# Kernel optimization log

Hardware: AMD Instinct MI355X
Metric: run time of the kernel (lower is better)

## Reference

```python
import jax, jax.numpy as jnp
import numpy as np

B = 8192
NUM_NODES = 100000
EMB = 128
W1D, W2D, W3D = 64, 128, 256   # witness_dims
CODE = 128
HID = 64                        # hardcoded hidden_dim in WitnessExtractor / decoder
TOTW = W1D + W2D + W3D          # 448


def _linear_params(key, fan_in, fan_out):
    k1, k2 = jax.random.split(key)
    bound = 1.0 / np.sqrt(fan_in)
    w = jax.random.uniform(k1, (fan_out, fan_in), jnp.float32, -bound, bound)
    b = jax.random.uniform(k2, (fan_out,), jnp.float32, -bound, bound)
    return w, b


def setup_inputs() -> dict:
    key = jax.random.key(0)
    ks = jax.random.split(key, 12)
    u = jax.random.randint(ks[0], (B,), 0, NUM_NODES, dtype=jnp.int64 if jax.config.jax_enable_x64 else jnp.int32)
    v = jax.random.randint(ks[1], (B,), 0, NUM_NODES, dtype=u.dtype)
    emb = jax.random.normal(ks[2], (NUM_NODES, EMB), jnp.float32)
    e1_w1, e1_b1 = _linear_params(ks[3], 2 * EMB, HID)
    e1_w2, e1_b2 = _linear_params(ks[4], HID, W1D)
    e2_w1, e2_b1 = _linear_params(ks[5], 2 * EMB + W1D, HID)
    e2_w2, e2_b2 = _linear_params(ks[6], HID, W2D)
    e3_w1, e3_b1 = _linear_params(ks[7], 2 * EMB + W2D, HID)
    e3_w2, e3_b2 = _linear_params(ks[8], HID, W3D)
    trop_w = jax.random.normal(ks[9], (CODE, TOTW), jnp.float32)  # init_scale=1.0
    dec_w1, dec_b1 = _linear_params(ks[10], CODE, HID)
    dec_w2, dec_b2 = _linear_params(ks[11], HID, 1)
    return dict(u=u, v=v, emb=emb,
                e1_w1=e1_w1, e1_b1=e1_b1, e1_w2=e1_w2, e1_b2=e1_b2,
                e2_w1=e2_w1, e2_b1=e2_b1, e2_w2=e2_w2, e2_b2=e2_b2,
                e3_w1=e3_w1, e3_b1=e3_b1, e3_w2=e3_w2, e3_b2=e3_b2,
                trop_w=trop_w, dec_w1=dec_w1, dec_b1=dec_b1,
                dec_w2=dec_w2, dec_b2=dec_b2)


def _witness(x, w1, b1, w2, b2):
    h = jax.nn.relu(x @ w1.T + b1)
    return jax.nn.sigmoid(h @ w2.T + b2)


def reference(u, v, emb,
              e1_w1, e1_b1, e1_w2, e1_b2,
              e2_w1, e2_b1, e2_w2, e2_b2,
              e3_w1, e3_b1, e3_w2, e3_b2,
              trop_w, dec_w1, dec_b1, dec_w2, dec_b2):
    u_emb = emb[u]                               # [B, EMB]
    v_emb = emb[v]
    base = jnp.concatenate([u_emb, v_emb], axis=1)  # [B, 2*EMB]
    w1 = _witness(base, e1_w1, e1_b1, e1_w2, e1_b2)
    w2 = _witness(jnp.concatenate([base, w1], axis=1), e2_w1, e2_b1, e2_w2, e2_b2)
    w3 = _witness(jnp.concatenate([base, w2], axis=1), e3_w1, e3_b1, e3_w2, e3_b2)
    wit = jnp.concatenate([w1, w2, w3], axis=1)  # [B, TOTW]
    # tropical (min-plus) matmul: code[b,o] = min_j (wit[b,j] + trop_w[o,j])
    code = jnp.min(wit[:, None, :] + trop_w[None, :, :], axis=2)  # [B, CODE]
    h = jax.nn.relu(code @ dec_w1.T + dec_b1)
    return h @ dec_w2.T + dec_b2                 # [B, 1]
```

## Files before the change

kernel.cpp:

```cpp
#include <hip/hip_runtime.h>
#include <hip/hip_fp16.h>
#include <math.h>

#define BATCH 8192
#define EMB 128
#define TILE 16
#define NTHREADS 1024
#define NWAVES 16
#define CH 136
#define SLOT 32

#define OFF_E1W1 0
#define OFF_E1W2 16384
#define OFF_E2W1 20480
#define OFF_E2W2 40960
#define OFF_E3W1 49152
#define OFF_E3W2 73728
#define OFF_DW1  90112
#define OFF_DW2  98304
#define W_DENSE  98368

typedef __attribute__((ext_vector_type(8))) _Float16 v8h;
typedef __attribute__((ext_vector_type(4))) float v4f;

struct Smem {
    _Float16 XB[32 * CH];
    _Float16 WC[56 * CH];
    _Float16 H[8 * CH];
    _Float16 CODE[16 * CH];
    unsigned int ent[128 * SLOT];
    unsigned int cnt[128];
};

__global__ __launch_bounds__(1024) void prep_kernel(
    const float* __restrict__ s0, const float* __restrict__ s1,
    const float* __restrict__ s2, const float* __restrict__ s3,
    const float* __restrict__ s4, const float* __restrict__ s5,
    const float* __restrict__ s6, const float* __restrict__ s7,
    const float* __restrict__ trop, _Float16* __restrict__ ws)
{
    const int b = blockIdx.x;
    const int tid = threadIdx.x;
    if (b < 25) {
        const int idx4 = (b * 1024 + tid) * 4;
        if (idx4 >= W_DENSE) return;
        const float* src; int off;
        if      (idx4 < OFF_E1W2) { src = s0; off = OFF_E1W1; }
        else if (idx4 < OFF_E2W1) { src = s1; off = OFF_E1W2; }
        else if (idx4 < OFF_E2W2) { src = s2; off = OFF_E2W1; }
        else if (idx4 < OFF_E3W1) { src = s3; off = OFF_E2W2; }
        else if (idx4 < OFF_E3W2) { src = s4; off = OFF_E3W1; }
        else if (idx4 < OFF_DW1)  { src = s5; off = OFF_E3W2; }
        else if (idx4 < OFF_DW2)  { src = s6; off = OFF_DW1;  }
        else                      { src = s7; off = OFF_DW2;  }
        const float4 v = *(const float4*)(src + (idx4 - off));
        _Float16* dst = ws + idx4;
        dst[0] = (_Float16)v.x; dst[1] = (_Float16)v.y;
        dst[2] = (_Float16)v.z; dst[3] = (_Float16)v.w;
    } else {
        const int lane = tid & 63;
        const int wave = tid >> 6;
        const int o = (b - 25) * 16 + wave;
        if (o >= 128) return;
        unsigned int* base = (unsigned int*)(ws + W_DENSE);

        const float* row = trop + (size_t)o * 448;
        float vals[7];
        float mn = 1e30f;
        #pragma unroll
        for (int it = 0; it < 7; ++it) {
            vals[it] = row[lane + it * 64];
            mn = fminf(mn, vals[it]);
        }
        mn = fminf(mn, __shfl_xor(mn, 1, 64));
        mn = fminf(mn, __shfl_xor(mn, 2, 64));
        mn = fminf(mn, __shfl_xor(mn, 4, 64));
        mn = fminf(mn, __shfl_xor(mn, 8, 64));
        mn = fminf(mn, __shfl_xor(mn, 16, 64));
        mn = fminf(mn, __shfl_xor(mn, 32, 64));
        const float thr = mn + 1.02f;

        const unsigned long long ltmask = (1ull << lane) - 1ull;
        unsigned int pos0 = 0;
        #pragma unroll
        for (int it = 0; it < 7; ++it) {
            const bool sel = vals[it] <= thr;
            const unsigned long long m = __ballot(sel);
            if (sel) {
                const unsigned int pos = pos0 + (unsigned)__popcll(m & ltmask);
                if (pos < SLOT) {
                    const unsigned short hb =
                        __builtin_bit_cast(unsigned short, (_Float16)vals[it]);
                    base[o * SLOT + pos] = ((unsigned)(lane + it * 64) << 16) | hb;
                }
            }
            pos0 += (unsigned)__popcll(m);
        }
        if (lane == 0) base[4096 + o] = pos0;
    }
}

template <int K, int O, int ACT>
__device__ __forceinline__ void dense_job(
    const _Float16* __restrict__ Wg, const float* __restrict__ bias,
    const _Float16* A0, _Float16* OutC, int jid, int lane)
{
    constexpr int STEPS = K / 32;
    static_assert(STEPS % 2 == 0, "even steps");
    const int l15 = lane & 15;
    const int quad = lane >> 4;
    const int o = jid * 16 + l15;
    const _Float16* wrow = Wg + (size_t)o * K + quad * 8;
    v4f c0 = {0.f, 0.f, 0.f, 0.f};
    v4f c1 = {0.f, 0.f, 0.f, 0.f};
    #pragma unroll
    for (int s = 0; s < STEPS; s += 2) {
        const v8h a0 = *(const v8h*)(A0 + (s * 4 + quad) * CH + l15 * 8);
        const v8h b0 = *(const v8h*)(wrow + s * 32);
        const v8h a1 = *(const v8h*)(A0 + ((s + 1) * 4 + quad) * CH + l15 * 8);
        const v8h b1 = *(const v8h*)(wrow + (s + 1) * 32);
        c0 = __builtin_amdgcn_mfma_f32_16x16x32_f16(a0, b0, c0, 0, 0, 0);
        c1 = __builtin_amdgcn_mfma_f32_16x16x32_f16(a1, b1, c1, 0, 0, 0);
    }
    const v4f c = c0 + c1;
    const float bs = bias[o];
    #pragma unroll
    for (int i = 0; i < 4; ++i) {
        float vv = c[i] + bs;
        if (ACT == 0) vv = fmaxf(vv, 0.f);
        else          vv = 1.f / (1.f + __expf(-vv));
        const int m = quad * 4 + i;
        OutC[(o >> 3) * CH + m * 8 + (o & 7)] = (_Float16)vv;
    }
}

template <int KW, int RS>
__device__ __forceinline__ void addpb_job(
    const _Float16* __restrict__ Wg, const _Float16* A0,
    const v4f hold, _Float16* OutH, int jid, int lane)
{
    constexpr int STEPS = KW / 32;
    static_assert(STEPS % 2 == 0, "even steps");
    const int l15 = lane & 15;
    const int quad = lane >> 4;
    const int o = jid * 16 + l15;
    const _Float16* wrow = Wg + (size_t)o * RS + quad * 8;
    v4f c0 = hold;
    v4f c1 = {0.f, 0.f, 0.f, 0.f};
    #pragma unroll
    for (int s = 0; s < STEPS; s += 2) {
        const v8h a0 = *(const v8h*)(A0 + (s * 4 + quad) * CH + l15 * 8);
        const v8h b0 = *(const v8h*)(wrow + s * 32);
        const v8h a1 = *(const v8h*)(A0 + ((s + 1) * 4 + quad) * CH + l15 * 8);
        const v8h b1 = *(const v8h*)(wrow + (s + 1) * 32);
        c0 = __builtin_amdgcn_mfma_f32_16x16x32_f16(a0, b0, c0, 0, 0, 0);
        c1 = __builtin_amdgcn_mfma_f32_16x16x32_f16(a1, b1, c1, 0, 0, 0);
    }
    const v4f c = c0 + c1;
    #pragma unroll
    for (int i = 0; i < 4; ++i) {
        const float vv = fmaxf(c[i], 0.f);
        const int m = quad * 4 + i;
        OutH[(o >> 3) * CH + m * 8 + (o & 7)] = (_Float16)vv;
    }
}

__global__ __launch_bounds__(NTHREADS, 8) void tacit_fused_kernel(
    const int* __restrict__ u, const int* __restrict__ v,
    const float* __restrict__ emb,
    const float* __restrict__ e1_b1, const float* __restrict__ e1_b2,
    const float* __restrict__ e2_b1, const float* __restrict__ e2_b2,
    const float* __restrict__ e3_b1, const float* __restrict__ e3_b2,
    const float* __restrict__ dec_b1, const float* __restrict__ dec_b2,
    const float* __restrict__ trop,
    const _Float16* __restrict__ ws,
    float* __restrict__ out)
{
    __shared__ Smem S;
    const int tid = threadIdx.x;
    const int lane = tid & 63;
    const int wave = tid >> 6;
    const int row0 = blockIdx.x * TILE;

    {
        const unsigned int* base = (const unsigned int*)(ws + W_DENSE);
        *(uint4*)&S.ent[tid * 4] = *(const uint4*)(base + tid * 4);
        if (tid < 32) *(uint4*)&S.cnt[tid * 4] = *(const uint4*)(base + 4096 + tid * 4);
    }
    if (tid < 512) {
        const int row = tid & 15;
        const int kq = tid >> 4;
        const int node = (kq < 16) ? u[row0 + row] : v[row0 + row];
        const int col = (kq & 15) * 8;
        const float4 f0 = *(const float4*)(emb + (size_t)node * EMB + col);
        const float4 f1 = *(const float4*)(emb + (size_t)node * EMB + col + 4);
        v8h hv;
        hv[0] = (_Float16)f0.x; hv[1] = (_Float16)f0.y;
        hv[2] = (_Float16)f0.z; hv[3] = (_Float16)f0.w;
        hv[4] = (_Float16)f1.x; hv[5] = (_Float16)f1.y;
        hv[6] = (_Float16)f1.z; hv[7] = (_Float16)f1.w;
        *(v8h*)&S.XB[kq * CH + row * 8] = hv;
    }
    __syncthreads();

    v4f hold = {0.f, 0.f, 0.f, 0.f};
    if (wave < 12) {
        const int tgt = wave >> 2;
        const int nt  = wave & 3;
        const int l15 = lane & 15;
        const int quad = lane >> 4;
        const int o = nt * 16 + l15;
        const _Float16* wrow;
        const float* bias;
        if (tgt == 0)      { wrow = ws + OFF_E1W1 + (size_t)o * 256; bias = e1_b1; }
        else if (tgt == 1) { wrow = ws + OFF_E2W1 + (size_t)o * 320; bias = e2_b1; }
        else               { wrow = ws + OFF_E3W1 + (size_t)o * 384; bias = e3_b1; }
        wrow += quad * 8;
        v4f c0 = {0.f, 0.f, 0.f, 0.f};
        v4f c1 = {0.f, 0.f, 0.f, 0.f};
        #pragma unroll
        for (int s = 0; s < 8; s += 2) {
            const v8h a0 = *(const v8h*)(S.XB + (s * 4 + quad) * CH + l15 * 8);
            const v8h b0 = *(const v8h*)(wrow + s * 32);
            const v8h a1 = *(const v8h*)(S.XB + ((s + 1) * 4 + quad) * CH + l15 * 8);
            const v8h b1v = *(const v8h*)(wrow + (s + 1) * 32);
            c0 = __builtin_amdgcn_mfma_f32_16x16x32_f16(a0, b0, c0, 0, 0, 0);
            c1 = __builtin_amdgcn_mfma_f32_16x16x32_f16(a1, b1v, c1, 0, 0, 0);
        }
        const v4f c = c0 + c1;
        const float bs = bias[o];
        if (tgt == 0) {
            #pragma unroll
            for (int i = 0; i < 4; ++i) {
                const float vv = fmaxf(c[i] + bs, 0.f);
                S.H[(o >> 3) * CH + (quad * 4 + i) * 8 + (o & 7)] = (_Float16)vv;
            }
        } else {
            #pragma unroll
            for (int i = 0; i < 4; ++i) hold[i] = c[i] + bs;
        }
    }
    __syncthreads();

    if (wave < 4)
        dense_job<64, 64, 1>(ws + OFF_E1W2, e1_b2, S.H, S.WC, wave, lane);
    __syncthreads();

    if (wave >= 4 && wave < 8)
        addpb_job<64, 320>(ws + OFF_E2W1 + 256, S.WC, hold, S.H, wave - 4, lane);
    __syncthreads();

    {
        const int dnt = (wave < 4) ? wave : (wave >= 12 ? wave - 8 : -1);
        if (dnt >= 0)
            dense_job<64, 128, 1>(ws + OFF_E2W2, e2_b2, S.H, S.WC + 8 * CH, dnt, lane);
    }
    __syncthreads();

    if (wave >= 8 && wave < 12)
        addpb_job<128, 384>(ws + OFF_E3W1 + 256, S.WC + 8 * CH, hold, S.H, wave - 8, lane);
    __syncthreads();

    dense_job<64, 256, 1>(ws + OFF_E3W2, e3_b2, S.H, S.WC + 24 * CH, wave, lane);
    __syncthreads();

    {
        const int r = lane & 15;
        const int cp = lane >> 4;
        const _Float16* wr8 = &S.WC[r * 8];
        float acc[8];
        int idx[8], end8[8];
        #pragma unroll
        for (int i = 0; i < 8; ++i) {
            const int o = (wave << 3) + i;
            const int n = (int)S.cnt[o];
            idx[i] = o * SLOT + cp;
            end8[i] = o * SLOT + (n < SLOT ? n : SLOT);
            acc[i] = 1e30f;
        }
        bool any = true;
        while (any) {
            any = false;
            #pragma unroll
            for (int i = 0; i < 8; ++i) {
                if (idx[i] < end8[i]) {
                    const unsigned int cwv = S.ent[idx[i]];
                    const int j = (int)(cwv >> 16);
                    const float tv = (float)__builtin_bit_cast(
                        _Float16, (unsigned short)(cwv & 0xffffu));
                    acc[i] = fminf(acc[i], (float)wr8[(j >> 3) * CH + (j & 7)] + tv);
                    idx[i] += 4;
                    any = true;
                }
            }
        }
        #pragma unroll
        for (int i = 0; i < 8; ++i) {
            const int o = (wave << 3) + i;
            if ((int)S.cnt[o] > SLOT) {
                const float* trow = trop + (size_t)o * 448;
                for (int j = cp; j < 448; j += 4)
                    acc[i] = fminf(acc[i], (float)wr8[(j >> 3) * CH + (j & 7)] + trow[j]);
            }
        }
        #pragma unroll
        for (int i = 0; i < 8; ++i) {
            float a = acc[i];
            a = fminf(a, __shfl_xor(a, 16, 64));
            a = fminf(a, __shfl_xor(a, 32, 64));
            if (cp == 0) {
                const int o = (wave << 3) + i;
                S.CODE[(o >> 3) * CH + r * 8 + (o & 7)] = (_Float16)a;
            }
        }
    }
    __syncthreads();

    if (wave < 4)
        dense_job<128, 64, 0>(ws + OFF_DW1, dec_b1, S.CODE, S.H, wave, lane);
    __syncthreads();

    if (tid < 64) {
        const int r = lane & 15;
        const int part = lane >> 4;
        const _Float16* w2 = ws + OFF_DW2;
        float s = 0.f;
        #pragma unroll
        for (int q = 0; q < 2; ++q) {
            const int c = part + q * 4;
            const v8h hr = *(const v8h*)(&S.H[c * CH + r * 8]);
            const v8h wr = *(const v8h*)(w2 + c * 8);
            #pragma unroll
            for (int t = 0; t < 8; ++t) s += (float)hr[t] * (float)wr[t];
        }
        s += __shfl_xor(s, 16, 64);
        s += __shfl_xor(s, 32, 64);
        if (part == 0) out[row0 + r] = s + dec_b2[0];
    }
}

extern "C" void kernel_launch(void* const* d_in, const int* in_sizes, int n_in,
                              void* d_out, int out_size, void* d_ws, size_t ws_size,
                              hipStream_t stream) {
    const int*   u      = (const int*)d_in[0];
    const int*   v      = (const int*)d_in[1];
    const float* emb    = (const float*)d_in[2];
    const float* e1_w1  = (const float*)d_in[3];
    const float* e1_b1  = (const float*)d_in[4];
    const float* e1_w2  = (const float*)d_in[5];
    const float* e1_b2  = (const float*)d_in[6];
    const float* e2_w1  = (const float*)d_in[7];
    const float* e2_b1  = (const float*)d_in[8];
    const float* e2_w2  = (const float*)d_in[9];
    const float* e2_b2  = (const float*)d_in[10];
    const float* e3_w1  = (const float*)d_in[11];
    const float* e3_b1  = (const float*)d_in[12];
    const float* e3_w2  = (const float*)d_in[13];
    const float* e3_b2  = (const float*)d_in[14];
    const float* trop_w = (const float*)d_in[15];
    const float* dec_w1 = (const float*)d_in[16];
    const float* dec_b1 = (const float*)d_in[17];
    const float* dec_w2 = (const float*)d_in[18];
    const float* dec_b2 = (const float*)d_in[19];
    float* out = (float*)d_out;
    _Float16* ws = (_Float16*)d_ws;

    prep_kernel<<<33, 1024, 0, stream>>>(
        e1_w1, e1_w2, e2_w1, e2_w2, e3_w1, e3_w2, dec_w1, dec_w2, trop_w, ws);

    tacit_fused_kernel<<<BATCH / TILE, NTHREADS, 0, stream>>>(
        u, v, emb,
        e1_b1, e1_b2, e2_b1, e2_b2, e3_b1, e3_b2, dec_b1, dec_b2,
        trop_w, ws, out);
}
```

Baseline: 151.5 us.

## Process two 16-row tiles per block and read sparse tropical entries from global

Each 1024-thread block now handles 32 batch rows as two 16-row sub-tiles, so waves that sat idle in the chained witness stages get work on the second tile. The grid is halved and the base GEMMs, dense jobs and decoder are redistributed across all 16 waves. The sparse tropical entry table is no longer staged into LDS and is read from global or L2 instead, and XB and CODE share a union to keep LDS size in check. The trade-off is more serial work per block, fewer blocks, and global-latency loads in the min-plus loop.

After: 163.9 us. +8.2%, slower.

```diff
diff --git a/kernel.cpp b/kernel.cpp
--- a/kernel.cpp
+++ b/kernel.cpp
@@ -4,7 +4,6 @@
 
 #define BATCH 8192
 #define EMB 128
-#define TILE 16
 #define NTHREADS 1024
 #define NWAVES 16
 #define CH 136
@@ -24,12 +23,12 @@
 typedef __attribute__((ext_vector_type(4))) float v4f;
 
 struct Smem {
-    _Float16 XB[32 * CH];
-    _Float16 WC[56 * CH];
-    _Float16 H[8 * CH];
-    _Float16 CODE[16 * CH];
-    unsigned int ent[128 * SLOT];
-    unsigned int cnt[128];
+    union {
+        _Float16 XB[2][32 * CH];
+        _Float16 CODE[2][16 * CH];
+    } U;
+    _Float16 WC[2][56 * CH];
+    _Float16 H[2][8 * CH];
 };
 
 __global__ __launch_bounds__(1024) void prep_kernel(
@@ -129,9 +128,40 @@
         float vv = c[i] + bs;
         if (ACT == 0) vv = fmaxf(vv, 0.f);
         else          vv = 1.f / (1.f + __expf(-vv));
-        const int m = quad * 4 + i;
-        OutC[(o >> 3) * CH + m * 8 + (o & 7)] = (_Float16)vv;
-    }
+        OutC[(o >> 3) * CH + (quad * 4 + i) * 8 + (o & 7)] = (_Float16)vv;
+    }
+}
+
+__device__ __forceinline__ v4f base_gemm(
+    const _Float16* __restrict__ ws, const _Float16* XB, int tgt, int nt,
+    int lane, const float* __restrict__ b1, const float* __restrict__ b2,
+    const float* __restrict__ b3)
+{
+    const int l15 = lane & 15;
+    const int quad = lane >> 4;
+    const int o = nt * 16 + l15;
+    const _Float16* wrow;
+    const float* bias;
+    if (tgt == 0)      { wrow = ws + OFF_E1W1 + (size_t)o * 256; bias = b1; }
+    else if (tgt == 1) { wrow = ws + OFF_E2W1 + (size_t)o * 320; bias = b2; }
+    else               { wrow = ws + OFF_E3W1 + (size_t)o * 384; bias = b3; }
+    wrow += quad * 8;
+    v4f c0 = {0.f, 0.f, 0.f, 0.f};
+    v4f c1 = {0.f, 0.f, 0.f, 0.f};
+    #pragma unroll
+    for (int s = 0; s < 8; s += 2) {
+        const v8h a0 = *(const v8h*)(XB + (s * 4 + quad) * CH + l15 * 8);
+        const v8h b0 = *(const v8h*)(wrow + s * 32);
+        const v8h a1 = *(const v8h*)(XB + ((s + 1) * 4 + quad) * CH + l15 * 8);
+        const v8h b1v = *(const v8h*)(wrow + (s + 1) * 32);
+        c0 = __builtin_amdgcn_mfma_f32_16x16x32_f16(a0, b0, c0, 0, 0, 0);
+        c1 = __builtin_amdgcn_mfma_f32_16x16x32_f16(a1, b1v, c1, 0, 0, 0);
+    }
+    v4f c = c0 + c1;
+    const float bs = bias[o];
+    #pragma unroll
+    for (int i = 0; i < 4; ++i) c[i] += bs;
+    return c;
 }
 
 template <int KW, int RS>
@@ -160,8 +190,7 @@
     #pragma unroll
     for (int i = 0; i < 4; ++i) {
         const float vv = fmaxf(c[i], 0.f);
-        const int m = quad * 4 + i;
-        OutH[(o >> 3) * CH + m * 8 + (o & 7)] = (_Float16)vv;
+        OutH[(o >> 3) * CH + (quad * 4 + i) * 8 + (o & 7)] = (_Float16)vv;
     }
 }
 
@@ -180,17 +209,14 @@
     const int tid = threadIdx.x;
     const int lane = tid & 63;
     const int wave = tid >> 6;
-    const int row0 = blockIdx.x * TILE;
+    const int row0 = blockIdx.x * 32;
 
     {
-        const unsigned int* base = (const unsigned int*)(ws + W_DENSE);
-        *(uint4*)&S.ent[tid * 4] = *(const uint4*)(base + tid * 4);
-        if (tid < 32) *(uint4*)&S.cnt[tid * 4] = *(const uint4*)(base + 4096 + tid * 4);
-    }
-    if (tid < 512) {
-        const int row = tid & 15;
-        const int kq = tid >> 4;
-        const int node = (kq < 16) ? u[row0 + row] : v[row0 + row];
+        const int t   = tid >> 9;
+        const int t9  = tid & 511;
+        const int row = t9 & 15;
+        const int kq  = t9 >> 4;
+        const int node = (kq < 16) ? u[row0 + t * 16 + row] : v[row0 + t * 16 + row];
         const int col = (kq & 15) * 8;
         const float4 f0 = *(const float4*)(emb + (size_t)node * EMB + col);
         const float4 f1 = *(const float4*)(emb + (size_t)node * EMB + col + 4);
@@ -199,128 +225,135 @@
         hv[2] = (_Float16)f0.z; hv[3] = (_Float16)f0.w;
         hv[4] = (_Float16)f1.x; hv[5] = (_Float16)f1.y;
         hv[6] = (_Float16)f1.z; hv[7] = (_Float16)f1.w;
-        *(v8h*)&S.XB[kq * CH + row * 8] = hv;
-    }
-    __syncthreads();
-
-    v4f hold = {0.f, 0.f, 0.f, 0.f};
-    if (wave < 12) {
-        const int tgt = wave >> 2;
-        const int nt  = wave & 3;
+        *(v8h*)&S.U.XB[t][kq * CH + row * 8] = hv;
+    }
+    __syncthreads();
+
+    v4f hold_a = {0.f, 0.f, 0.f, 0.f};
+    v4f hold_b = {0.f, 0.f, 0.f, 0.f};
+    {
         const int l15 = lane & 15;
         const int quad = lane >> 4;
-        const int o = nt * 16 + l15;
-        const _Float16* wrow;
-        const float* bias;
-        if (tgt == 0)      { wrow = ws + OFF_E1W1 + (size_t)o * 256; bias = e1_b1; }
-        else if (tgt == 1) { wrow = ws + OFF_E2W1 + (size_t)o * 320; bias = e2_b1; }
-        else               { wrow = ws + OFF_E3W1 + (size_t)o * 384; bias = e3_b1; }
-        wrow += quad * 8;
-        v4f c0 = {0.f, 0.f, 0.f, 0.f};
-        v4f c1 = {0.f, 0.f, 0.f, 0.f};
-        #pragma unroll
-        for (int s = 0; s < 8; s += 2) {
-            const v8h a0 = *(const v8h*)(S.XB + (s * 4 + quad) * CH + l15 * 8);
-            const v8h b0 = *(const v8h*)(wrow + s * 32);
-            const v8h a1 = *(const v8h*)(S.XB + ((s + 1) * 4 + quad) * CH + l15 * 8);
-            const v8h b1v = *(const v8h*)(wrow + (s + 1) * 32);
-            c0 = __builtin_amdgcn_mfma_f32_16x16x32_f16(a0, b0, c0, 0, 0, 0);
-            c1 = __builtin_amdgcn_mfma_f32_16x16x32_f16(a1, b1v, c1, 0, 0, 0);
-        }
-        const v4f c = c0 + c1;
-        const float bs = bias[o];
-        if (tgt == 0) {
+        if (wave < 12) {
+            const int tgt = wave >> 2;
+            const v4f c = base_gemm(ws, S.U.XB[0], tgt, wave & 3, lane,
+                                    e1_b1, e2_b1, e3_b1);
+            if (tgt == 0) {
+                const int o = (wave & 3) * 16 + l15;
+                #pragma unroll
+                for (int i = 0; i < 4; ++i)
+                    S.H[0][(o >> 3) * CH + (quad * 4 + i) * 8 + (o & 7)] =
+                        (_Float16)fmaxf(c[i], 0.f);
+            } else {
+                hold_a = c;
+            }
+        } else {
+            const v4f c = base_gemm(ws, S.U.XB[1], 0, wave & 3, lane,
+                                    e1_b1, e2_b1, e3_b1);
+            const int o = (wave & 3) * 16 + l15;
             #pragma unroll
-            for (int i = 0; i < 4; ++i) {
-                const float vv = fmaxf(c[i] + bs, 0.f);
-                S.H[(o >> 3) * CH + (quad * 4 + i) * 8 + (o & 7)] = (_Float16)vv;
-            }
-        } else {
-            #pragma unroll
-            for (int i = 0; i < 4; ++i) hold[i] = c[i] + bs;
-        }
-    }
-    __syncthreads();
-
-    if (wave < 4)
-        dense_job<64, 64, 1>(ws + OFF_E1W2, e1_b2, S.H, S.WC, wave, lane);
+            for (int i = 0; i < 4; ++i)
+                S.H[1][(o >> 3) * CH + (quad * 4 + i) * 8 + (o & 7)] =
+                    (_Float16)fmaxf(c[i], 0.f);
+        }
+        if (wave < 8) {
+            hold_b = base_gemm(ws, S.U.XB[1], (wave >> 2) + 1, wave & 3, lane,
+                               e1_b1, e2_b1, e3_b1);
+        }
+    }
+    __syncthreads();
+
+    if (wave >= 8)
+        dense_job<64, 64, 1>(ws + OFF_E1W2, e1_b2, S.H[(wave - 8) >> 2],
+                             S.WC[(wave - 8) >> 2], (wave - 8) & 3, lane);
     __syncthreads();
 
     if (wave >= 4 && wave < 8)
-        addpb_job<64, 320>(ws + OFF_E2W1 + 256, S.WC, hold, S.H, wave - 4, lane);
+        addpb_job<64, 320>(ws + OFF_E2W1 + 256, S.WC[0], hold_a, S.H[0], wave - 4, lane);
+    else if (wave < 4)
+        addpb_job<64, 320>(ws + OFF_E2W1 + 256, S.WC[1], hold_b, S.H[1], wave, lane);
+    __syncthreads();
+
+    dense_job<64, 128, 1>(ws + OFF_E2W2, e2_b2, S.H[wave >> 3],
+                          S.WC[wave >> 3] + 8 * CH, wave & 7, lane);
+    __syncthreads();
+
+    if (wave >= 8 && wave < 12)
+        addpb_job<128, 384>(ws + OFF_E3W1 + 256, S.WC[0] + 8 * CH, hold_a,
+                            S.H[0], wave - 8, lane);
+    else if (wave >= 4 && wave < 8)
+        addpb_job<128, 384>(ws + OFF_E3W1 + 256, S.WC[1] + 8 * CH, hold_b,
+                            S.H[1], wave - 4, lane);
+    __syncthreads();
+
+    dense_job<64, 256, 1>(ws + OFF_E3W2, e3_b2, S.H[0], S.WC[0] + 24 * CH, wave, lane);
+    dense_job<64, 256, 1>(ws + OFF_E3W2, e3_b2, S.H[1], S.WC[1] + 24 * CH, wave, lane);
     __syncthreads();
 
     {
-        const int dnt = (wave < 4) ? wave : (wave >= 12 ? wave - 8 : -1);
-        if (dnt >= 0)
-            dense_job<64, 128, 1>(ws + OFF_E2W2, e2_b2, S.H, S.WC + 8 * CH, dnt, lane);
-    }
-    __syncthreads();
-
-    if (wave >= 8 && wave < 12)
-        addpb_job<128, 384>(ws + OFF_E3W1 + 256, S.WC + 8 * CH, hold, S.H, wave - 8, lane);
-    __syncthreads();
-
-    dense_job<64, 256, 1>(ws + OFF_E3W2, e3_b2, S.H, S.WC + 24 * CH, wave, lane);
-    __syncthreads();
-
-    {
+        const unsigned int* entg = (const unsigned int*)(ws + W_DENSE);
+        const unsigned int* cntg = entg + 4096;
         const int r = lane & 15;
         const int cp = lane >> 4;
-        const _Float16* wr8 = &S.WC[r * 8];
-        float acc[8];
-        int idx[8], end8[8];
-        #pragma unroll
-        for (int i = 0; i < 8; ++i) {
-            const int o = (wave << 3) + i;
-            const int n = (int)S.cnt[o];
-            idx[i] = o * SLOT + cp;
-            end8[i] = o * SLOT + (n < SLOT ? n : SLOT);
-            acc[i] = 1e30f;
-        }
-        bool any = true;
-        while (any) {
-            any = false;
+        #pragma unroll 1
+        for (int t = 0; t < 2; ++t) {
+            const _Float16* wr8 = &S.WC[t][r * 8];
+            float acc[8];
+            int idx8[8], end8[8];
             #pragma unroll
             for (int i = 0; i < 8; ++i) {
-                if (idx[i] < end8[i]) {
-                    const unsigned int cwv = S.ent[idx[i]];
-                    const int j = (int)(cwv >> 16);
-                    const float tv = (float)__builtin_bit_cast(
-                        _Float16, (unsigned short)(cwv & 0xffffu));
-                    acc[i] = fminf(acc[i], (float)wr8[(j >> 3) * CH + (j & 7)] + tv);
-                    idx[i] += 4;
-                    any = true;
+                const int o = (wave << 3) + i;
+                const int n = (int)cntg[o];
+                idx8[i] = o * SLOT + cp;
+                end8[i] = o * SLOT + (n < SLOT ? n : SLOT);
+                acc[i] = 1e30f;
+            }
+            bool any = true;
+            while (any) {
+                any = false;
+                #pragma unroll
+                for (int i = 0; i < 8; ++i) {
+                    if (idx8[i] < end8[i]) {
+                        const unsigned int cwv = entg[idx8[i]];
+                        const int j = (int)(cwv >> 16);
+                        const float tv = (float)__builtin_bit_cast(
+                            _Float16, (unsigned short)(cwv & 0xffffu));
+                        acc[i] = fminf(acc[i], (float)wr8[(j >> 3) * CH + (j & 7)] + tv);
+                        idx8[i] += 4;
+                        any = true;
+                    }
                 }
             }
-        }
-        #pragma unroll
-        for (int i = 0; i < 8; ++i) {
-            const int o = (wave << 3) + i;
-            if ((int)S.cnt[o] > SLOT) {
-                const float* trow = trop + (size_t)o * 448;
-                for (int j = cp; j < 448; j += 4)
-                    acc[i] = fminf(acc[i], (float)wr8[(j >> 3) * CH + (j & 7)] + trow[j]);
-            }
-        }
-        #pragma unroll
-        for (int i = 0; i < 8; ++i) {
-            float a = acc[i];
-            a = fminf(a, __shfl_xor(a, 16, 64));
-            a = fminf(a, __shfl_xor(a, 32, 64));
-            if (cp == 0) {
+            #pragma unroll
+            for (int i = 0; i < 8; ++i) {
                 const int o = (wave << 3) + i;
-                S.CODE[(o >> 3) * CH + r * 8 + (o & 7)] = (_Float16)a;
-            }
-        }
-    }
-    __syncthreads();
-
-    if (wave < 4)
-        dense_job<128, 64, 0>(ws + OFF_DW1, dec_b1, S.CODE, S.H, wave, lane);
-    __syncthreads();
-
-    if (tid < 64) {
+                if ((int)cntg[o] > SLOT) {
+                    const float* trow = trop + (size_t)o * 448;
+                    for (int j = cp; j < 448; j += 4)
+                        acc[i] = fminf(acc[i],
+                                       (float)wr8[(j >> 3) * CH + (j & 7)] + trow[j]);
+                }
+            }
+            #pragma unroll
+            for (int i = 0; i < 8; ++i) {
+                float a = acc[i];
+                a = fminf(a, __shfl_xor(a, 16, 64));
+                a = fminf(a, __shfl_xor(a, 32, 64));
+                if (cp == 0) {
+                    const int o = (wave << 3) + i;
+                    S.U.CODE[t][(o >> 3) * CH + r * 8 + (o & 7)] = (_Float16)a;
+                }
+            }
+        }
+    }
+    __syncthreads();
+
+    if (wave < 8)
+        dense_job<128, 64, 0>(ws + OFF_DW1, dec_b1, S.U.CODE[wave >> 2],
+                              S.H[wave >> 2], wave & 3, lane);
+    __syncthreads();
+
+    if (wave < 2) {
         const int r = lane & 15;
         const int part = lane >> 4;
         const _Float16* w2 = ws + OFF_DW2;
@@ -328,14 +361,14 @@
         #pragma unroll
         for (int q = 0; q < 2; ++q) {
             const int c = part + q * 4;
-            const v8h hr = *(const v8h*)(&S.H[c * CH + r * 8]);
+            const v8h hr = *(const v8h*)(&S.H[wave][c * CH + r * 8]);
             const v8h wr = *(const v8h*)(w2 + c * 8);
             #pragma unroll
             for (int t = 0; t < 8; ++t) s += (float)hr[t] * (float)wr[t];
         }
         s += __shfl_xor(s, 16, 64);
         s += __shfl_xor(s, 32, 64);
-        if (part == 0) out[row0 + r] = s + dec_b2[0];
+        if (part == 0) out[row0 + wave * 16 + r] = s + dec_b2[0];
     }
 }
 
@@ -368,7 +401,7 @@
     prep_kernel<<<33, 1024, 0, stream>>>(
         e1_w1, e1_w2, e2_w1, e2_w2, e3_w1, e3_w2, dec_w1, dec_w2, trop_w, ws);
 
-    tacit_fused_kernel<<<BATCH / TILE, NTHREADS, 0, stream>>>(
+    tacit_fused_kernel<<<BATCH / 32, NTHREADS, 0, stream>>>(
         u, v, emb,
         e1_b1, e1_b2, e2_b1, e2_b2, e3_b1, e3_b2, dec_b1, dec_b2,
         trop_w, ws, out);
```

## Drop prep kernel and build sparse tropical table inside fused kernel

Applied to the files above, without the earlier changes.

Removes the separate prep launch: each block now builds the pruned tropical-weight entry list itself, spreading the row builds across waves that are idle during the witness MLP stages. Dense weights are read as fp32 and converted to fp16 on the fly instead of from a prebuilt fp16 workspace. The XB and CODE buffers share LDS through a union. This trades a kernel launch and its serial dependency for redundant per-block trop reads from L2 and extra conversion work in the GEMM loops.

Result: slower. 172.0 us (+13.5%).

```diff
diff --git a/kernel.cpp b/kernel.cpp
--- a/kernel.cpp
+++ b/kernel.cpp
@@ -10,99 +10,73 @@
 #define CH 136
 #define SLOT 32
 
-#define OFF_E1W1 0
-#define OFF_E1W2 16384
-#define OFF_E2W1 20480
-#define OFF_E2W2 40960
-#define OFF_E3W1 49152
-#define OFF_E3W2 73728
-#define OFF_DW1  90112
-#define OFF_DW2  98304
-#define W_DENSE  98368
-
 typedef __attribute__((ext_vector_type(8))) _Float16 v8h;
 typedef __attribute__((ext_vector_type(4))) float v4f;
 
 struct Smem {
-    _Float16 XB[32 * CH];
+    union {
+        _Float16 XB[32 * CH];
+        _Float16 CODE[16 * CH];
+    } U;
     _Float16 WC[56 * CH];
     _Float16 H[8 * CH];
-    _Float16 CODE[16 * CH];
     unsigned int ent[128 * SLOT];
     unsigned int cnt[128];
 };
 
-__global__ __launch_bounds__(1024) void prep_kernel(
-    const float* __restrict__ s0, const float* __restrict__ s1,
-    const float* __restrict__ s2, const float* __restrict__ s3,
-    const float* __restrict__ s4, const float* __restrict__ s5,
-    const float* __restrict__ s6, const float* __restrict__ s7,
-    const float* __restrict__ trop, _Float16* __restrict__ ws)
-{
-    const int b = blockIdx.x;
-    const int tid = threadIdx.x;
-    if (b < 25) {
-        const int idx4 = (b * 1024 + tid) * 4;
-        if (idx4 >= W_DENSE) return;
-        const float* src; int off;
-        if      (idx4 < OFF_E1W2) { src = s0; off = OFF_E1W1; }
-        else if (idx4 < OFF_E2W1) { src = s1; off = OFF_E1W2; }
-        else if (idx4 < OFF_E2W2) { src = s2; off = OFF_E2W1; }
-        else if (idx4 < OFF_E3W1) { src = s3; off = OFF_E2W2; }
-        else if (idx4 < OFF_E3W2) { src = s4; off = OFF_E3W1; }
-        else if (idx4 < OFF_DW1)  { src = s5; off = OFF_E3W2; }
-        else if (idx4 < OFF_DW2)  { src = s6; off = OFF_DW1;  }
-        else                      { src = s7; off = OFF_DW2;  }
-        const float4 v = *(const float4*)(src + (idx4 - off));
-        _Float16* dst = ws + idx4;
-        dst[0] = (_Float16)v.x; dst[1] = (_Float16)v.y;
-        dst[2] = (_Float16)v.z; dst[3] = (_Float16)v.w;
-    } else {
-        const int lane = tid & 63;
-        const int wave = tid >> 6;
-        const int o = (b - 25) * 16 + wave;
-        if (o >= 128) return;
-        unsigned int* base = (unsigned int*)(ws + W_DENSE);
-
-        const float* row = trop + (size_t)o * 448;
-        float vals[7];
-        float mn = 1e30f;
-        #pragma unroll
-        for (int it = 0; it < 7; ++it) {
-            vals[it] = row[lane + it * 64];
-            mn = fminf(mn, vals[it]);
-        }
-        mn = fminf(mn, __shfl_xor(mn, 1, 64));
-        mn = fminf(mn, __shfl_xor(mn, 2, 64));
-        mn = fminf(mn, __shfl_xor(mn, 4, 64));
-        mn = fminf(mn, __shfl_xor(mn, 8, 64));
-        mn = fminf(mn, __shfl_xor(mn, 16, 64));
-        mn = fminf(mn, __shfl_xor(mn, 32, 64));
-        const float thr = mn + 1.02f;
-
-        const unsigned long long ltmask = (1ull << lane) - 1ull;
-        unsigned int pos0 = 0;
-        #pragma unroll
-        for (int it = 0; it < 7; ++it) {
-            const bool sel = vals[it] <= thr;
-            const unsigned long long m = __ballot(sel);
-            if (sel) {
-                const unsigned int pos = pos0 + (unsigned)__popcll(m & ltmask);
-                if (pos < SLOT) {
-                    const unsigned short hb =
-                        __builtin_bit_cast(unsigned short, (_Float16)vals[it]);
-                    base[o * SLOT + pos] = ((unsigned)(lane + it * 64) << 16) | hb;
-                }
+__device__ __forceinline__ v8h load8f(const float* __restrict__ p) {
+    const float4 a = *(const float4*)p;
+    const float4 b = *(const float4*)(p + 4);
+    v8h r;
+    r[0] = (_Float16)a.x; r[1] = (_Float16)a.y;
+    r[2] = (_Float16)a.z; r[3] = (_Float16)a.w;
+    r[4] = (_Float16)b.x; r[5] = (_Float16)b.y;
+    r[6] = (_Float16)b.z; r[7] = (_Float16)b.w;
+    return r;
+}
+
+__device__ __forceinline__ void build_row(
+    const float* __restrict__ trop, int o, int lane,
+    unsigned int* __restrict__ ent, unsigned int* __restrict__ cnt)
+{
+    const float* row = trop + (size_t)o * 448;
+    float vals[7];
+    float mn = 1e30f;
+    #pragma unroll
+    for (int it = 0; it < 7; ++it) {
+        vals[it] = row[lane + it * 64];
+        mn = fminf(mn, vals[it]);
+    }
+    mn = fminf(mn, __shfl_xor(mn, 1, 64));
+    mn = fminf(mn, __shfl_xor(mn, 2, 64));
+    mn = fminf(mn, __shfl_xor(mn, 4, 64));
+    mn = fminf(mn, __shfl_xor(mn, 8, 64));
+    mn = fminf(mn, __shfl_xor(mn, 16, 64));
+    mn = fminf(mn, __shfl_xor(mn, 32, 64));
+    const float thr = mn + 1.02f;
+
+    const unsigned long long ltmask = (1ull << lane) - 1ull;
+    unsigned int pos0 = 0;
+    #pragma unroll
+    for (int it = 0; it < 7; ++it) {
+        const bool sel = vals[it] <= thr;
+        const unsigned long long m = __ballot(sel);
+        if (sel) {
+            const unsigned int pos = pos0 + (unsigned)__popcll(m & ltmask);
+            if (pos < SLOT) {
+                const unsigned short hb =
+                    __builtin_bit_cast(unsigned short, (_Float16)vals[it]);
+                ent[o * SLOT + pos] = ((unsigned)(lane + it * 64) << 16) | hb;
             }
-            pos0 += (unsigned)__popcll(m);
-        }
-        if (lane == 0) base[4096 + o] = pos0;
-    }
-}
-
-template <int K, int O, int ACT>
+        }
+        pos0 += (unsigned)__popcll(m);
+    }
+    if (lane == 0) cnt[o] = pos0;
+}
+
+template <int K, int ACT>
 __device__ __forceinline__ void dense_job(
-    const _Float16* __restrict__ Wg, const float* __restrict__ bias,
+    const float* __restrict__ Wg, const float* __restrict__ bias,
     const _Float16* A0, _Float16* OutC, int jid, int lane)
 {
     constexpr int STEPS = K / 32;
@@ -110,15 +84,15 @@
     const int l15 = lane & 15;
     const int quad = lane >> 4;
     const int o = jid * 16 + l15;
-    const _Float16* wrow = Wg + (size_t)o * K + quad * 8;
+    const float* wrow = Wg + (size_t)o * K + quad * 8;
     v4f c0 = {0.f, 0.f, 0.f, 0.f};
     v4f c1 = {0.f, 0.f, 0.f, 0.f};
     #pragma unroll
     for (int s = 0; s < STEPS; s += 2) {
         const v8h a0 = *(const v8h*)(A0 + (s * 4 + quad) * CH + l15 * 8);
-        const v8h b0 = *(const v8h*)(wrow + s * 32);
+        const v8h b0 = load8f(wrow + s * 32);
         const v8h a1 = *(const v8h*)(A0 + ((s + 1) * 4 + quad) * CH + l15 * 8);
-        const v8h b1 = *(const v8h*)(wrow + (s + 1) * 32);
+        const v8h b1 = load8f(wrow + (s + 1) * 32);
         c0 = __builtin_amdgcn_mfma_f32_16x16x32_f16(a0, b0, c0, 0, 0, 0);
         c1 = __builtin_amdgcn_mfma_f32_16x16x32_f16(a1, b1, c1, 0, 0, 0);
     }
@@ -129,14 +103,47 @@
         float vv = c[i] + bs;
         if (ACT == 0) vv = fmaxf(vv, 0.f);
         else          vv = 1.f / (1.f + __expf(-vv));
-        const int m = quad * 4 + i;
-        OutC[(o >> 3) * CH + m * 8 + (o & 7)] = (_Float16)vv;
-    }
+        OutC[(o >> 3) * CH + (quad * 4 + i) * 8 + (o & 7)] = (_Float16)vv;
+    }
+}
+
+__device__ __forceinline__ v4f base_gemm(
+    const _Float16* XB, int tgt, int nt, int lane,
+    const float* __restrict__ w1g, const float* __restrict__ w2g,
+    const float* __restrict__ w3g,
+    const float* __restrict__ b1, const float* __restrict__ b2,
+    const float* __restrict__ b3)
+{
+    const int l15 = lane & 15;
+    const int quad = lane >> 4;
+    const int o = nt * 16 + l15;
+    const float* wrow;
+    const float* bias;
+    if (tgt == 0)      { wrow = w1g + (size_t)o * 256; bias = b1; }
+    else if (tgt == 1) { wrow = w2g + (size_t)o * 320; bias = b2; }
+    else               { wrow = w3g + (size_t)o * 384; bias = b3; }
+    wrow += quad * 8;
+    v4f c0 = {0.f, 0.f, 0.f, 0.f};
+    v4f c1 = {0.f, 0.f, 0.f, 0.f};
+    #pragma unroll
+    for (int s = 0; s < 8; s += 2) {
+        const v8h a0 = *(const v8h*)(XB + (s * 4 + quad) * CH + l15 * 8);
+        const v8h b0 = load8f(wrow + s * 32);
+        const v8h a1 = *(const v8h*)(XB + ((s + 1) * 4 + quad) * CH + l15 * 8);
+        const v8h b1v = load8f(wrow + (s + 1) * 32);
+        c0 = __builtin_amdgcn_mfma_f32_16x16x32_f16(a0, b0, c0, 0, 0, 0);
+        c1 = __builtin_amdgcn_mfma_f32_16x16x32_f16(a1, b1v, c1, 0, 0, 0);
+    }
+    v4f c = c0 + c1;
+    const float bs = bias[o];
+    #pragma unroll
+    for (int i = 0; i < 4; ++i) c[i] += bs;
+    return c;
 }
 
 template <int KW, int RS>
 __device__ __forceinline__ void addpb_job(
-    const _Float16* __restrict__ Wg, const _Float16* A0,
+    const float* __restrict__ Wg, const _Float16* A0,
     const v4f hold, _Float16* OutH, int jid, int lane)
 {
     constexpr int STEPS = KW / 32;
@@ -144,15 +151,15 @@
     const int l15 = lane & 15;
     const int quad = lane >> 4;
     const int o = jid * 16 + l15;
-    const _Float16* wrow = Wg + (size_t)o * RS + quad * 8;
+    const float* wrow = Wg + (size_t)o * RS + quad * 8;
     v4f c0 = hold;
     v4f c1 = {0.f, 0.f, 0.f, 0.f};
     #pragma unroll
     for (int s = 0; s < STEPS; s += 2) {
         const v8h a0 = *(const v8h*)(A0 + (s * 4 + quad) * CH + l15 * 8);
-        const v8h b0 = *(const v8h*)(wrow + s * 32);
+        const v8h b0 = load8f(wrow + s * 32);
         const v8h a1 = *(const v8h*)(A0 + ((s + 1) * 4 + quad) * CH + l15 * 8);
-        const v8h b1 = *(const v8h*)(wrow + (s + 1) * 32);
+        const v8h b1 = load8f(wrow + (s + 1) * 32);
         c0 = __builtin_amdgcn_mfma_f32_16x16x32_f16(a0, b0, c0, 0, 0, 0);
         c1 = __builtin_amdgcn_mfma_f32_16x16x32_f16(a1, b1, c1, 0, 0, 0);
     }
@@ -160,20 +167,22 @@
     #pragma unroll
     for (int i = 0; i < 4; ++i) {
         const float vv = fmaxf(c[i], 0.f);
-        const int m = quad * 4 + i;
-        OutH[(o >> 3) * CH + m * 8 + (o & 7)] = (_Float16)vv;
+        OutH[(o >> 3) * CH + (quad * 4 + i) * 8 + (o & 7)] = (_Float16)vv;
     }
 }
 
 __global__ __launch_bounds__(NTHREADS, 8) void tacit_fused_kernel(
     const int* __restrict__ u, const int* __restrict__ v,
     const float* __restrict__ emb,
-    const float* __restrict__ e1_b1, const float* __restrict__ e1_b2,
-    const float* __restrict__ e2_b1, const float* __restrict__ e2_b2,
-    const float* __restrict__ e3_b1, const float* __restrict__ e3_b2,
-    const float* __restrict__ dec_b1, const float* __restrict__ dec_b2,
+    const float* __restrict__ e1_w1, const float* __restrict__ e1_b1,
+    const float* __restrict__ e1_w2, const float* __restrict__ e1_b2,
+    const float* __restrict__ e2_w1, const float* __restrict__ e2_b1,
+    const float* __restrict__ e2_w2, const float* __restrict__ e2_b2,
+    const float* __restrict__ e3_w1, const float* __restrict__ e3_b1,
+    const float* __restrict__ e3_w2, const float* __restrict__ e3_b2,
     const float* __restrict__ trop,
-    const _Float16* __restrict__ ws,
+    const float* __restrict__ dec_w1, const float* __restrict__ dec_b1,
+    const float* __restrict__ dec_w2, const float* __restrict__ dec_b2,
     float* __restrict__ out)
 {
     __shared__ Smem S;
@@ -182,11 +191,6 @@
     const int wave = tid >> 6;
     const int row0 = blockIdx.x * TILE;
 
-    {
-        const unsigned int* base = (const unsigned int*)(ws + W_DENSE);
-        *(uint4*)&S.ent[tid * 4] = *(const uint4*)(base + tid * 4);
-        if (tid < 32) *(uint4*)&S.cnt[tid * 4] = *(const uint4*)(base + 4096 + tid * 4);
-    }
     if (tid < 512) {
         const int row = tid & 15;
         const int kq = tid >> 4;
@@ -199,69 +203,71 @@
         hv[2] = (_Float16)f0.z; hv[3] = (_Float16)f0.w;
         hv[4] = (_Float16)f1.x; hv[5] = (_Float16)f1.y;
         hv[6] = (_Float16)f1.z; hv[7] = (_Float16)f1.w;
-        *(v8h*)&S.XB[kq * CH + row * 8] = hv;
-    }
-    __syncthreads();
-
-    v4f hold = {0.f, 0.f, 0.f, 0.f};
+        *(v8h*)&S.U.XB[kq * CH + row * 8] = hv;
+    } else {
+        const int b0r = (wave - 8) * 2;
+        build_row(trop, b0r,     lane, S.ent, S.cnt);
+        build_row(trop, b0r + 1, lane, S.ent, S.cnt);
+    }
+    __syncthreads();
+
+    v4f hold2 = {0.f, 0.f, 0.f, 0.f};
+    v4f hold3 = {0.f, 0.f, 0.f, 0.f};
     if (wave < 12) {
         const int tgt = wave >> 2;
-        const int nt  = wave & 3;
-        const int l15 = lane & 15;
-        const int quad = lane >> 4;
-        const int o = nt * 16 + l15;
-        const _Float16* wrow;
-        const float* bias;
-        if (tgt == 0)      { wrow = ws + OFF_E1W1 + (size_t)o * 256; bias = e1_b1; }
-        else if (tgt == 1) { wrow = ws + OFF_E2W1 + (size_t)o * 320; bias = e2_b1; }
-        else               { wrow = ws + OFF_E3W1 + (size_t)o * 384; bias = e3_b1; }
-        wrow += quad * 8;
-        v4f c0 = {0.f, 0.f, 0.f, 0.f};
-        v4f c1 = {0.f, 0.f, 0.f, 0.f};
-        #pragma unroll
-        for (int s = 0; s < 8; s += 2) {
-            const v8h a0 = *(const v8h*)(S.XB + (s * 4 + quad) * CH + l15 * 8);
-            const v8h b0 = *(const v8h*)(wrow + s * 32);
-            const v8h a1 = *(const v8h*)(S.XB + ((s + 1) * 4 + quad) * CH + l15 * 8);
-            const v8h b1v = *(const v8h*)(wrow + (s + 1) * 32);
-            c0 = __builtin_amdgcn_mfma_f32_16x16x32_f16(a0, b0, c0, 0, 0, 0);
-            c1 = __builtin_amdgcn_mfma_f32_16x16x32_f16(a1, b1v, c1, 0, 0, 0);
-        }
-        const v4f c = c0 + c1;
-        const float bs = bias[o];
+        const v4f c = base_gemm(S.U.XB, tgt, wave & 3, lane,
+                                e1_w1, e2_w1, e3_w1, e1_b1, e2_b1, e3_b1);
         if (tgt == 0) {
+            const int l15 = lane & 15;
+            const int quad = lane >> 4;
+            const int o = (wave & 3) * 16 + l15;
             #pragma unroll
-            for (int i = 0; i < 4; ++i) {
-                const float vv = fmaxf(c[i] + bs, 0.f);
-                S.H[(o >> 3) * CH + (quad * 4 + i) * 8 + (o & 7)] = (_Float16)vv;
-            }
+            for (int i = 0; i < 4; ++i)
+                S.H[(o >> 3) * CH + (quad * 4 + i) * 8 + (o & 7)] =
+                    (_Float16)fmaxf(c[i], 0.f);
+        } else if (tgt == 1) {
+            hold2 = c;
         } else {
-            #pragma unroll
-            for (int i = 0; i < 4; ++i) hold[i] = c[i] + bs;
-        }
-    }
-    __syncthreads();
-
-    if (wave < 4)
-        dense_job<64, 64, 1>(ws + OFF_E1W2, e1_b2, S.H, S.WC, wave, lane);
-    __syncthreads();
-
-    if (wave >= 4 && wave < 8)
-        addpb_job<64, 320>(ws + OFF_E2W1 + 256, S.WC, hold, S.H, wave - 4, lane);
+            hold3 = c;
+        }
+    } else {
+        const int b0r = 16 + (wave - 12) * 4;
+        #pragma unroll
+        for (int t = 0; t < 4; ++t) build_row(trop, b0r + t, lane, S.ent, S.cnt);
+    }
+    __syncthreads();
+
+    if (wave < 4) {
+        dense_job<64, 1>(e1_w2, e1_b2, S.H, S.WC, wave, lane);
+    } else {
+        const int b0r = 32 + (wave - 4) * 4;
+        #pragma unroll
+        for (int t = 0; t < 4; ++t) build_row(trop, b0r + t, lane, S.ent, S.cnt);
+    }
+    __syncthreads();
+
+    if (wave >= 4 && wave < 8) {
+        addpb_job<64, 320>(e2_w1 + 256, S.WC, hold2, S.H, wave - 4, lane);
+    } else {
+        const int idx = (wave < 4) ? wave : (wave - 4);
+        const int b0r = 80 + idx * 4;
+        #pragma unroll
+        for (int t = 0; t < 4; ++t) build_row(trop, b0r + t, lane, S.ent, S.cnt);
+    }
     __syncthreads();
 
     {
         const int dnt = (wave < 4) ? wave : (wave >= 12 ? wave - 8 : -1);
         if (dnt >= 0)
-            dense_job<64, 128, 1>(ws + OFF_E2W2, e2_b2, S.H, S.WC + 8 * CH, dnt, lane);
+            dense_job<64, 1>(e2_w2, e2_b2, S.H, S.WC + 8 * CH, dnt, lane);
     }
     __syncthreads();
 
     if (wave >= 8 && wave < 12)
-        addpb_job<128, 384>(ws + OFF_E3W1 + 256, S.WC + 8 * CH, hold, S.H, wave - 8, lane);
-    __syncthreads();
-
-    dense_job<64, 256, 1>(ws + OFF_E3W2, e3_b2, S.H, S.WC + 24 * CH, wave, lane);
+        addpb_job<128, 384>(e3_w1 + 256, S.WC + 8 * CH, hold3, S.H, wave - 8, lane);
+    __syncthreads();
+
+    dense_job<64, 1>(e3_w2, e3_b2, S.H, S.WC + 24 * CH, wave, lane);
     __syncthreads();
 
     {
@@ -269,12 +275,12 @@
         const int cp = lane >> 4;
         const _Float16* wr8 = &S.WC[r * 8];
         float acc[8];
-        int idx[8], end8[8];
+        int idx8[8], end8[8];
         #pragma unroll
         for (int i = 0; i < 8; ++i) {
             const int o = (wave << 3) + i;
             const int n = (int)S.cnt[o];
-            idx[i] = o * SLOT + cp;
+            idx8[i] = o * SLOT + cp;
             end8[i] = o * SLOT + (n < SLOT ? n : SLOT);
             acc[i] = 1e30f;
         }
@@ -283,13 +289,13 @@
             any = false;
             #pragma unroll
             for (int i = 0; i < 8; ++i) {
-                if (idx[i] < end8[i]) {
-                    const unsigned int cwv = S.ent[idx[i]];
+                if (idx8[i] < end8[i]) {
+                    const unsigned int cwv = S.ent[idx8[i]];
                     const int j = (int)(cwv >> 16);
                     const float tv = (float)__builtin_bit_cast(
                         _Float16, (unsigned short)(cwv & 0xffffu));
                     acc[i] = fminf(acc[i], (float)wr8[(j >> 3) * CH + (j & 7)] + tv);
-                    idx[i] += 4;
+                    idx8[i] += 4;
                     any = true;
                 }
             }
@@ -300,7 +306,8 @@
             if ((int)S.cnt[o] > SLOT) {
                 const float* trow = trop + (size_t)o * 448;
                 for (int j = cp; j < 448; j += 4)
-                    acc[i] = fminf(acc[i], (float)wr8[(j >> 3) * CH + (j & 7)] + trow[j]);
+                    acc[i] = fminf(acc[i],
+                                   (float)wr8[(j >> 3) * CH + (j & 7)] + trow[j]);
             }
         }
         #pragma unroll
@@ -310,28 +317,30 @@
             a = fminf(a, __shfl_xor(a, 32, 64));
             if (cp == 0) {
                 const int o = (wave << 3) + i;
-                S.CODE[(o >> 3) * CH + r * 8 + (o & 7)] = (_Float16)a;
+                S.U.CODE[(o >> 3) * CH + r * 8 + (o & 7)] = (_Float16)a;
             }
         }
     }
     __syncthreads();
 
     if (wave < 4)
-        dense_job<128, 64, 0>(ws + OFF_DW1, dec_b1, S.CODE, S.H, wave, lane);
+        dense_job<128, 0>(dec_w1, dec_b1, S.U.CODE, S.H, wave, lane);
     __syncthreads();
 
     if (tid < 64) {
         const int r = lane & 15;
         const int part = lane >> 4;
-        const _Float16* w2 = ws + OFF_DW2;
         float s = 0.f;
         #pragma unroll
         for (int q = 0; q < 2; ++q) {
             const int c = part + q * 4;
             const v8h hr = *(const v8h*)(&S.H[c * CH + r * 8]);
-            const v8h wr = *(const v8h*)(w2 + c * 8);
-            #pragma unroll
-            for (int t = 0; t < 8; ++t) s += (float)hr[t] * (float)wr[t];
+            const float4 w0 = *(const float4*)(dec_w2 + c * 8);
+            const float4 w1 = *(const float4*)(dec_w2 + c * 8 + 4);
+            s += (float)hr[0] * w0.x + (float)hr[1] * w0.y
+               + (float)hr[2] * w0.z + (float)hr[3] * w0.w
+               + (float)hr[4] * w1.x + (float)hr[5] * w1.y
+               + (float)hr[6] * w1.z + (float)hr[7] * w1.w;
         }
         s += __shfl_xor(s, 16, 64);
         s += __shfl_xor(s, 32, 64);
@@ -363,13 +372,13 @@
     const float* dec_w2 = (const float*)d_in[18];
     const float* dec_b2 = (const float*)d_in[19];
     float* out = (float*)d_out;
-    _Float16* ws = (_Float16*)d_ws;
-
-    prep_kernel<<<33, 1024, 0, stream>>>(
-        e1_w1, e1_w2, e2_w1, e2_w2, e3_w1, e3_w2, dec_w1, dec_w2, trop_w, ws);
+    (void)d_ws; (void)ws_size;
 
     tacit_fused_kernel<<<BATCH / TILE, NTHREADS, 0, stream>>>(
         u, v, emb,
-        e1_b1, e1_b2, e2_b1, e2_b2, e3_b1, e3_b2, dec_b1, dec_b2,
-        trop_w, ws, out);
-}
+        e1_w1, e1_b1, e1_w2, e1_b2,
+        e2_w1, e2_b1, e2_w2, e2_b2,
+        e3_w1, e3_b1, e3_w2, e3_b2,
+        trop_w, dec_w1, dec_b1, dec_w2, dec_b2,
+        out);
+}
```
